# Performance work log

Measured on AMD Instinct MI355X. Metric: run time of the kernel, lower is better.

The kernel has to match this reference:

```python
import jax, jax.numpy as jnp
import numpy as np

K_NN = 10  # k in the source

def setup_inputs() -> dict:
    key = jax.random.key(0)
    k1, k2, k3, k4, k5 = jax.random.split(key, 5)
    bs, N, d, n_concepts, n_classes = 4096, 200000, 256, 32, 10
    return {
        "train_embedding": jax.random.normal(k1, (bs, d), dtype=jnp.float32),
        "train_embeddings": jax.random.normal(k2, (N, d), dtype=jnp.float32),
        # init_concept: uniform in [-0.5, 0.5]
        "concept": jax.random.uniform(k3, (d, n_concepts), dtype=jnp.float32, minval=-0.5, maxval=0.5),
        "W_hx": jax.random.normal(k4, (d, n_classes), dtype=jnp.float32) * 0.05,
        "b_hx": jax.random.normal(k5, (n_classes,), dtype=jnp.float32) * 0.05,
    }


def reference(train_embedding, train_embeddings, concept, W_hx, b_hx):
    # concept: [d, nc]; train_embeddings: [N, d]; train_embedding: [bs, d]
    n_concepts = concept.shape[1]

    def h_x(z):  # linear classifier standing in for h_x
        return z @ W_hx + b_hx

    gram = concept.T @ concept                                # [nc, nc]
    proj_matrix = concept @ jnp.linalg.inv(gram) @ concept.T  # [d, d]
    proj = train_embedding @ proj_matrix.T                    # (proj_matrix @ X^T)^T, [bs, d]
    y_pred = h_x(proj)
    orig_pred = h_x(train_embedding)

    # Batched cdist across all concepts (replaces the per-concept python loop):
    # dist[n, j] = || train_embeddings[n] - concept[:, j] ||
    x2 = jnp.sum(train_embeddings * train_embeddings, axis=1, keepdims=True)  # [N, 1]
    c2 = jnp.sum(concept * concept, axis=0)                                   # [nc]
    xc = train_embeddings @ concept                                           # [N, nc]
    dist = jnp.sqrt(jnp.maximum(x2 + c2 - 2.0 * xc, 0.0))                     # [N, nc]

    # top-k SMALLEST distances per concept
    _, knn_idx = jax.lax.top_k(-dist.T, K_NN)          # [nc, k]
    knn = train_embeddings[knn_idx]                    # [nc, k, d] gather

    # L_sparse_1: mean over concepts of sum(c * c_knn) / k
    dots = jnp.einsum("dj,jkd->j", concept, knn) / K_NN   # [nc]
    L_sparse_1_new = jnp.mean(dots)

    eye = jnp.eye(n_concepts, dtype=gram.dtype)
    L_sparse_2_new = jnp.mean(gram * (1.0 - eye))
    norm_metrics = jnp.mean(gram * eye)

    return (orig_pred, y_pred, L_sparse_1_new, L_sparse_2_new, norm_metrics)
```

## Files before the change

### kernel.cpp

```cpp
#include <hip/hip_runtime.h>
#include <cstdint>

#define D 256
#define NC 32
#define NCLS 10
#define KNN 10
#define KROWS 128
#define CTS 260

typedef float f32x4 __attribute__((ext_vector_type(4)));
typedef float f4v __attribute__((ext_vector_type(4)));
typedef short short8v __attribute__((ext_vector_type(8)));

__device__ __forceinline__ float wave_sum(float v) {
  #pragma unroll
  for (int off = 32; off; off >>= 1) v += __shfl_xor(v, off);
  return v;
}

__device__ __forceinline__ uint32_t fbits(float x) { return __builtin_bit_cast(uint32_t, x); }
__device__ __forceinline__ float bcast(uint32_t b) { return __builtin_bit_cast(float, b); }

__global__ __launch_bounds__(512, 4) void k_key(const float* __restrict__ X,
                                                const float* __restrict__ C,
                                                float* __restrict__ candK,
                                                int* __restrict__ candI,
                                                int N, int G) {
  __shared__ uint4 shm[2048];
  int t = threadIdx.x;
  int lane = t & 63;
  int wvu = __builtin_amdgcn_readfirstlane(t >> 6);
  int rowbase = blockIdx.x * KROWS;

  #pragma unroll
  for (int e0 = 0; e0 < 1024; e0 += 512) {
    int e = e0 + t;
    int q = e >> 6, l = e & 63;
    int tile = q >> 3, ksq = q & 7;
    int col = tile * 16 + (l & 15), kg = (l >> 4) & 3;
    uint32_t h[8], lo[8];
    #pragma unroll
    for (int i = 0; i < 8; ++i) {
      int k = ksq * 32 + kg * 8 + i;
      float x = C[(size_t)k * NC + col];
      uint32_t hb = fbits(x) & 0xFFFF0000u;
      h[i] = hb >> 16;
      lo[i] = fbits(x - bcast(hb)) >> 16;
    }
    shm[e] = make_uint4((h[1] << 16) | h[0], (h[3] << 16) | h[2],
                        (h[5] << 16) | h[4], (h[7] << 16) | h[6]);
    shm[1024 + e] = make_uint4((lo[1] << 16) | lo[0], (lo[3] << 16) | lo[2],
                               (lo[5] << 16) | lo[4], (lo[7] << 16) | lo[6]);
  }
  __syncthreads();

  int r16 = lane & 15;
  int grow = rowbase + wvu * 16 + r16; if (grow >= N) grow = N - 1;
  const float* xp = X + (size_t)grow * D + ((lane >> 4) * 8);

  f32x4 aH0, aM0, aH1, aM1;
  #pragma unroll
  for (int i = 0; i < 4; ++i) { aH0[i] = 0.f; aM0[i] = 0.f; aH1[i] = 0.f; aM1[i] = 0.f; }
  float x2 = 0.f;

  #pragma unroll
  for (int ks = 0; ks < 8; ++ks) {
    f4v xa = __builtin_nontemporal_load(reinterpret_cast<const f4v*>(xp + ks * 32));
    f4v xb = __builtin_nontemporal_load(reinterpret_cast<const f4v*>(xp + ks * 32 + 4));
    float xs[8] = {xa[0], xa[1], xa[2], xa[3], xb[0], xb[1], xb[2], xb[3]};
    uint32_t hp[4], lp[4];
    #pragma unroll
    for (int p = 0; p < 4; ++p) {
      float x0 = xs[2 * p], x1 = xs[2 * p + 1];
      x2 = fmaf(x0, x0, x2); x2 = fmaf(x1, x1, x2);
      uint32_t h0 = fbits(x0) & 0xFFFF0000u, h1 = fbits(x1) & 0xFFFF0000u;
      hp[p] = h1 | (h0 >> 16);
      float r0 = x0 - bcast(h0), r1 = x1 - bcast(h1);
      lp[p] = (fbits(r1) & 0xFFFF0000u) | (fbits(r0) >> 16);
    }
    short8v xh = __builtin_bit_cast(short8v, make_uint4(hp[0], hp[1], hp[2], hp[3]));
    short8v xl = __builtin_bit_cast(short8v, make_uint4(lp[0], lp[1], lp[2], lp[3]));
    short8v b0h = __builtin_bit_cast(short8v, shm[ks * 64 + lane]);
    short8v b1h = __builtin_bit_cast(short8v, shm[(8 + ks) * 64 + lane]);
    short8v b0l = __builtin_bit_cast(short8v, shm[1024 + ks * 64 + lane]);
    short8v b1l = __builtin_bit_cast(short8v, shm[1024 + (8 + ks) * 64 + lane]);
    aH0 = __builtin_amdgcn_mfma_f32_16x16x32_bf16(xh, b0h, aH0, 0, 0, 0);
    aM0 = __builtin_amdgcn_mfma_f32_16x16x32_bf16(xh, b0l, aM0, 0, 0, 0);
    aM0 = __builtin_amdgcn_mfma_f32_16x16x32_bf16(xl, b0h, aM0, 0, 0, 0);
    aH1 = __builtin_amdgcn_mfma_f32_16x16x32_bf16(xh, b1h, aH1, 0, 0, 0);
    aM1 = __builtin_amdgcn_mfma_f32_16x16x32_bf16(xh, b1l, aM1, 0, 0, 0);
    aM1 = __builtin_amdgcn_mfma_f32_16x16x32_bf16(xl, b1h, aM1, 0, 0, 0);
  }

  x2 += __shfl_xor(x2, 16);
  x2 += __shfl_xor(x2, 32);

  __syncthreads();
  float* klb = reinterpret_cast<float*>(shm);
  #pragma unroll
  for (int i = 0; i < 4; ++i) {
    int m = (lane >> 4) * 4 + i;
    float x2m = __shfl(x2, m);
    int rowl = wvu * 16 + m;
    klb[rowl * 33 + r16]      = fmaf(-2.f, aH0[i] + aM0[i], x2m);
    klb[rowl * 33 + 16 + r16] = fmaf(-2.f, aH1[i] + aM1[i], x2m);
  }
  __syncthreads();

  {
    int c = t >> 4, sub = t & 15;
    const float INF = 3.4e38f;
    float bk[8]; int bi[8];
    #pragma unroll
    for (int q = 0; q < 8; ++q) { bk[q] = INF; bi[q] = 0x7fffffff; }
    #pragma unroll
    for (int rr = 0; rr < 8; ++rr) {
      int rowl = sub * 8 + rr;
      int gi = rowbase + rowl;
      float v = (gi < N) ? klb[rowl * 33 + c] : INF;
      float cv = v; int ci = gi;
      #pragma unroll
      for (int q = 0; q < 8; ++q) {
        bool take = (cv < bk[q]) || (cv == bk[q] && ci < bi[q]);
        if (take) {
          float tf = bk[q]; bk[q] = cv; cv = tf;
          int ti = bi[q]; bi[q] = ci; ci = ti;
        }
      }
    }
    #pragma unroll
    for (int r = 0; r < KNN; ++r) {
      float mv = bk[0]; int mgi = bi[0];
      #pragma unroll
      for (int off = 1; off < 16; off <<= 1) {
        float ov = __shfl_xor(mv, off); int oi = __shfl_xor(mgi, off);
        if (ov < mv || (ov == mv && oi < mgi)) { mv = ov; mgi = oi; }
      }
      bool won = (bk[0] == mv) && (bi[0] == mgi);
      #pragma unroll
      for (int q = 0; q < 7; ++q) {
        bk[q] = won ? bk[q + 1] : bk[q];
        bi[q] = won ? bi[q + 1] : bi[q];
      }
      if (won) { bk[7] = INF; bi[7] = 0x7fffffff; }
      if (sub == 0) {
        candK[((size_t)c * G + blockIdx.x) * KNN + r] = mv;
        candI[((size_t)c * G + blockIdx.x) * KNN + r] = mgi;
      }
    }
  }
}

#define AUGW (NC + NCLS)
__global__ __launch_bounds__(1024) void k_gramsolve(const float* __restrict__ C,
                                                    const float* __restrict__ W,
                                                    float* __restrict__ T2,
                                                    float* __restrict__ out, int bs) {
  __shared__ float T[(NC + NCLS) * CTS];
  __shared__ float aug[NC * AUGW];
  __shared__ float Ssh[NC * NCLS];
  int tid = threadIdx.x;

  const float4* C4 = (const float4*)C;
  for (int s = tid; s < 2048; s += 1024) {
    float4 v = C4[s];
    int d = s >> 3, c0 = (s & 7) * 4;
    T[(c0 + 0) * CTS + d] = v.x; T[(c0 + 1) * CTS + d] = v.y;
    T[(c0 + 2) * CTS + d] = v.z; T[(c0 + 3) * CTS + d] = v.w;
  }
  const float2* W2 = (const float2*)W;
  for (int s = tid; s < 1280; s += 1024) {
    float2 v = W2[s];
    int d = s / 5, c0 = (s % 5) * 2;
    T[(NC + c0) * CTS + d] = v.x; T[(NC + c0 + 1) * CTS + d] = v.y;
  }
  __syncthreads();

  int lane = tid & 63, wv = tid >> 6;
  #pragma unroll
  for (int half = 0; half < 2; ++half) {
    int i = wv + half * 16;
    if (lane < AUGW) {
      const float4* ri = (const float4*)&T[i * CTS];
      const float4* rj = (const float4*)&T[lane * CTS];
      float acc = 0.f;
      #pragma unroll 8
      for (int d4 = 0; d4 < 64; ++d4) {
        float4 a = ri[d4], b = rj[d4];
        acc += a.x * b.x + a.y * b.y + a.z * b.z + a.w * b.w;
      }
      aug[i * AUGW + lane] = acc;
    }
  }
  __syncthreads();

  if (tid < NC) {
    int l2 = tid;
    float row[AUGW];
    #pragma unroll
    for (int c = 0; c < AUGW; ++c) row[c] = aug[l2 * AUGW + c];

    float rsum = 0.f;
    #pragma unroll
    for (int c = 0; c < NC; ++c) rsum += row[c];
    float diag = row[l2];
    #pragma unroll
    for (int off = 16; off; off >>= 1) {
      rsum += __shfl_xor(rsum, off);
      diag += __shfl_xor(diag, off);
    }
    if (l2 == 0) {
      out[(size_t)2 * bs * NCLS + 1] = (rsum - diag) / (float)(NC * NC);
      out[(size_t)2 * bs * NCLS + 2] = diag / (float)(NC * NC);
      out[(size_t)2 * bs * NCLS] = 0.f;
    }

    for (int k = 0; k < NC; ++k) {
      float prow[AUGW];
      #pragma unroll
      for (int c = 0; c < AUGW; ++c) prow[c] = __shfl(row[c], k);
      float pinv = 1.0f / prow[k];
      float f = row[k] * pinv;
      if (l2 == k) {
        #pragma unroll
        for (int c = 0; c < AUGW; ++c) row[c] *= pinv;
      } else {
        #pragma unroll
        for (int c = 0; c < AUGW; ++c) row[c] -= f * prow[c];
      }
    }
    #pragma unroll
    for (int c = 0; c < NCLS; ++c) Ssh[l2 * NCLS + c] = row[NC + c];
  }
  __syncthreads();

  for (int e = tid; e < D * NCLS; e += 1024) {
    int d = e / NCLS, cls = e % NCLS;
    float acc = 0.f;
    #pragma unroll
    for (int c = 0; c < NC; ++c) acc += T[c * CTS + d] * Ssh[c * NCLS + cls];
    T2[e] = acc;
  }
}

__global__ __launch_bounds__(256) void k_pred(const float* __restrict__ X,
                                              const float* __restrict__ W,
                                              const float* __restrict__ T2,
                                              const float* __restrict__ bvec,
                                              float* __restrict__ out, int bs) {
  __shared__ float2 Ws2[1280];
  __shared__ float2 Ts2[1280];
  int t = threadIdx.x;
  const float2* W2 = (const float2*)W;
  const float2* T22 = (const float2*)T2;
  for (int s = t; s < 1280; s += 256) { Ws2[s] = W2[s]; Ts2[s] = T22[s]; }
  __syncthreads();

  int r = blockIdx.x * 8 + (t >> 5);
  int q = t & 31;
  const float4* x4 = reinterpret_cast<const float4*>(X + (size_t)r * D);
  float4 xa = x4[q * 2], xb = x4[q * 2 + 1];

  float o[NCLS], y[NCLS];
  #pragma unroll
  for (int c = 0; c < NCLS; ++c) { o[c] = 0.f; y[c] = 0.f; }

  #pragma unroll
  for (int i = 0; i < 8; ++i) {
    int d = q * 8 + i;
    float xd = (i < 4) ? reinterpret_cast<const float*>(&xa)[i]
                       : reinterpret_cast<const float*>(&xb)[i - 4];
    #pragma unroll
    for (int j = 0; j < 5; ++j) {
      float2 wv = Ws2[d * 5 + j];
      float2 tv = Ts2[d * 5 + j];
      o[j * 2 + 0] += xd * wv.x; o[j * 2 + 1] += xd * wv.y;
      y[j * 2 + 0] += xd * tv.x; y[j * 2 + 1] += xd * tv.y;
    }
  }
  #pragma unroll
  for (int off = 1; off < 32; off <<= 1) {
    #pragma unroll
    for (int c = 0; c < NCLS; ++c) {
      o[c] += __shfl_xor(o[c], off);
      y[c] += __shfl_xor(y[c], off);
    }
  }
  if (q < NCLS) {
    float b = bvec[q];
    out[(size_t)r * NCLS + q] = o[q] + b;
    out[(size_t)bs * NCLS + (size_t)r * NCLS + q] = y[q] + b;
  }
}

__global__ __launch_bounds__(512) void k_final(const float* __restrict__ candK,
                                               const int* __restrict__ candI,
                                               const float* __restrict__ X,
                                               const float* __restrict__ Cc,
                                               float* __restrict__ out, int bs, int G) {
  int j = blockIdx.x, tid = threadIdx.x;
  int M = G * KNN;
  const float INF = 3.4e38f;

  float bk[KNN]; int bi[KNN];
  #pragma unroll
  for (int q = 0; q < KNN; ++q) { bk[q] = INF; bi[q] = 0x7fffffff; }
  for (int e = tid; e < M; e += 512) {
    float v = candK[(size_t)j * M + e];
    int gi = candI[(size_t)j * M + e];
    if (v < bk[KNN - 1] || (v == bk[KNN - 1] && gi < bi[KNN - 1])) {
      float cv = v; int ci = gi;
      #pragma unroll
      for (int q = 0; q < KNN; ++q) {
        bool take = (cv < bk[q]) || (cv == bk[q] && ci < bi[q]);
        if (take) {
          float tf = bk[q]; bk[q] = cv; cv = tf;
          int ti = bi[q]; bi[q] = ci; ci = ti;
        }
      }
    }
  }

  __shared__ float sk[512 * KNN];
  __shared__ int si[512 * KNN];
  __shared__ float wv_[8]; __shared__ int wi_[8];
  __shared__ int topIdx[KNN];
  #pragma unroll
  for (int q = 0; q < KNN; ++q) { sk[tid * KNN + q] = bk[q]; si[tid * KNN + q] = bi[q]; }
  __syncthreads();

  int p = 0;
  int lane = tid & 63, wv = tid >> 6;
  for (int rr = 0; rr < KNN; ++rr) {
    float myv = (p < KNN) ? sk[tid * KNN + p] : INF;
    int mygi = (p < KNN) ? si[tid * KNN + p] : 0x7fffffff;
    float hv = myv; int hgi = mygi;
    #pragma unroll
    for (int off = 32; off; off >>= 1) {
      float ov = __shfl_xor(hv, off); int oi = __shfl_xor(hgi, off);
      if (ov < hv || (ov == hv && oi < hgi)) { hv = ov; hgi = oi; }
    }
    if (lane == 0) { wv_[wv] = hv; wi_[wv] = hgi; }
    __syncthreads();
    float bv = wv_[0]; int bgi = wi_[0];
    #pragma unroll
    for (int w = 1; w < 8; ++w) {
      if (wv_[w] < bv || (wv_[w] == bv && wi_[w] < bgi)) { bv = wv_[w]; bgi = wi_[w]; }
    }
    if (p < KNN && myv == bv && mygi == bgi) p++;
    if (tid == 0) topIdx[rr] = bgi;
    __syncthreads();
  }

  if (tid < 256) {
    float cj = Cc[tid * NC + j];
    float acc = 0.f;
    #pragma unroll
    for (int k = 0; k < KNN; ++k) acc += X[(size_t)topIdx[k] * D + tid] * cj;
    acc = wave_sum(acc);
    __shared__ float rsum[4];
    if (lane == 0) rsum[wv] = acc;
    __syncthreads();
    if (tid == 0)
      atomicAdd(out + (size_t)2 * bs * NCLS,
                (rsum[0] + rsum[1] + rsum[2] + rsum[3]) * (1.0f / (KNN * NC)));
  }
}

extern "C" void kernel_launch(void* const* d_in, const int* in_sizes, int n_in,
                              void* d_out, int out_size, void* d_ws, size_t ws_size,
                              hipStream_t stream) {
  const float* Xb = (const float*)d_in[0];
  const float* XN = (const float*)d_in[1];
  const float* C  = (const float*)d_in[2];
  const float* W  = (const float*)d_in[3];
  const float* bv = (const float*)d_in[4];
  float* out = (float*)d_out;

  int bs = in_sizes[0] / D;
  int N  = in_sizes[1] / D;
  int G  = (N + KROWS - 1) / KROWS;

  float* w = (float*)d_ws;
  size_t offT2   = 0;
  size_t offCK   = 2560;
  size_t offCI   = offCK + (size_t)NC * G * KNN;

  float* T2    = w + offT2;
  float* candK = w + offCK;
  int*   candI = (int*)(w + offCI);

  k_key<<<dim3(G), dim3(512), 0, stream>>>(XN, C, candK, candI, N, G);
  k_gramsolve<<<dim3(1), dim3(1024), 0, stream>>>(C, W, T2, out, bs);
  k_pred<<<dim3(bs / 8), dim3(256), 0, stream>>>(Xb, W, T2, bv, out, bs);
  k_final<<<dim3(NC), dim3(512), 0, stream>>>(candK, candI, XN, C, out, bs, G);
}
```

Measured before the change: 165.3 us.

## Precompute concept bf16 split once and stage rows via async global-to-LDS loads

The bf16 hi/lo split of the concept matrix moves into the single-block gramsolve kernel, which now runs first and writes it to workspace. k_key loads it straight into registers instead of rebuilding it in every block. k_key now streams 32 rows per block into XOR-swizzled LDS with global_load_lds, and splits the 32 concept columns across wave pairs in 256-thread blocks. The candidate count rises to G≈6250 blocks with top-10 taken from 32 rows each, which enlarges the candidate lists the final kernel must merge. It also serialises gramsolve ahead of k_key.

```diff
diff --git a/kernel.cpp b/kernel.cpp
--- a/kernel.cpp
+++ b/kernel.cpp
@@ -5,12 +5,13 @@
 #define NC 32
 #define NCLS 10
 #define KNN 10
-#define KROWS 128
+#define KROWS 32
 #define CTS 260
 
 typedef float f32x4 __attribute__((ext_vector_type(4)));
-typedef float f4v __attribute__((ext_vector_type(4)));
 typedef short short8v __attribute__((ext_vector_type(8)));
+typedef const __attribute__((address_space(1))) unsigned int* gp1_t;
+typedef __attribute__((address_space(3))) unsigned int* sp3_t;
 
 __device__ __forceinline__ float wave_sum(float v) {
   #pragma unroll
@@ -21,53 +22,51 @@
 __device__ __forceinline__ uint32_t fbits(float x) { return __builtin_bit_cast(uint32_t, x); }
 __device__ __forceinline__ float bcast(uint32_t b) { return __builtin_bit_cast(float, b); }
 
-__global__ __launch_bounds__(512, 4) void k_key(const float* __restrict__ X,
-                                                const float* __restrict__ C,
+__global__ __launch_bounds__(256, 4) void k_key(const float* __restrict__ X,
+                                                const uint4* __restrict__ Fhi,
+                                                const uint4* __restrict__ Flo,
                                                 float* __restrict__ candK,
                                                 int* __restrict__ candI,
                                                 int N, int G) {
-  __shared__ uint4 shm[2048];
+  __shared__ float4 xf4[32 * 64];
   int t = threadIdx.x;
   int lane = t & 63;
   int wvu = __builtin_amdgcn_readfirstlane(t >> 6);
+  int tile = wvu & 1, rg = wvu >> 1;
   int rowbase = blockIdx.x * KROWS;
 
   #pragma unroll
-  for (int e0 = 0; e0 < 1024; e0 += 512) {
-    int e = e0 + t;
-    int q = e >> 6, l = e & 63;
-    int tile = q >> 3, ksq = q & 7;
-    int col = tile * 16 + (l & 15), kg = (l >> 4) & 3;
-    uint32_t h[8], lo[8];
-    #pragma unroll
-    for (int i = 0; i < 8; ++i) {
-      int k = ksq * 32 + kg * 8 + i;
-      float x = C[(size_t)k * NC + col];
-      uint32_t hb = fbits(x) & 0xFFFF0000u;
-      h[i] = hb >> 16;
-      lo[i] = fbits(x - bcast(hb)) >> 16;
-    }
-    shm[e] = make_uint4((h[1] << 16) | h[0], (h[3] << 16) | h[2],
-                        (h[5] << 16) | h[4], (h[7] << 16) | h[6]);
-    shm[1024 + e] = make_uint4((lo[1] << 16) | lo[0], (lo[3] << 16) | lo[2],
-                               (lo[5] << 16) | lo[4], (lo[7] << 16) | lo[6]);
-  }
-  __syncthreads();
-
-  int r16 = lane & 15;
-  int grow = rowbase + wvu * 16 + r16; if (grow >= N) grow = N - 1;
-  const float* xp = X + (size_t)grow * D + ((lane >> 4) * 8);
-
-  f32x4 aH0, aM0, aH1, aM1;
-  #pragma unroll
-  for (int i = 0; i < 4; ++i) { aH0[i] = 0.f; aM0[i] = 0.f; aH1[i] = 0.f; aM1[i] = 0.f; }
+  for (int j = 0; j < 8; ++j) {
+    int row = wvu * 8 + j;
+    int gr = rowbase + row; if (gr >= N) gr = N - 1;
+    const float* src = X + (size_t)gr * D + ((lane ^ (row & 15)) * 4);
+    __builtin_amdgcn_global_load_lds((gp1_t)(const void*)src,
+        (sp3_t)(void*)(&xf4[row * 64]), 16, 0, 0);
+  }
+
+  uint4 fh[8], fl[8];
+  #pragma unroll
+  for (int ks = 0; ks < 8; ++ks) {
+    fh[ks] = Fhi[(tile * 8 + ks) * 64 + lane];
+    fl[ks] = Flo[(tile * 8 + ks) * 64 + lane];
+  }
+
+  __syncthreads();
+
+  int r16 = lane & 15, kg = lane >> 4;
+  int rl = rg * 16 + r16;
+
+  f32x4 aH, aM;
+  #pragma unroll
+  for (int i = 0; i < 4; ++i) { aH[i] = 0.f; aM[i] = 0.f; }
   float x2 = 0.f;
 
   #pragma unroll
   for (int ks = 0; ks < 8; ++ks) {
-    f4v xa = __builtin_nontemporal_load(reinterpret_cast<const f4v*>(xp + ks * 32));
-    f4v xb = __builtin_nontemporal_load(reinterpret_cast<const f4v*>(xp + ks * 32 + 4));
-    float xs[8] = {xa[0], xa[1], xa[2], xa[3], xb[0], xb[1], xb[2], xb[3]};
+    int s0 = ks * 8 + kg * 2;
+    float4 xa = xf4[rl * 64 + (s0 ^ r16)];
+    float4 xb = xf4[rl * 64 + ((s0 + 1) ^ r16)];
+    float xs[8] = {xa.x, xa.y, xa.z, xa.w, xb.x, xb.y, xb.z, xb.w};
     uint32_t hp[4], lp[4];
     #pragma unroll
     for (int p = 0; p < 4; ++p) {
@@ -80,47 +79,41 @@
     }
     short8v xh = __builtin_bit_cast(short8v, make_uint4(hp[0], hp[1], hp[2], hp[3]));
     short8v xl = __builtin_bit_cast(short8v, make_uint4(lp[0], lp[1], lp[2], lp[3]));
-    short8v b0h = __builtin_bit_cast(short8v, shm[ks * 64 + lane]);
-    short8v b1h = __builtin_bit_cast(short8v, shm[(8 + ks) * 64 + lane]);
-    short8v b0l = __builtin_bit_cast(short8v, shm[1024 + ks * 64 + lane]);
-    short8v b1l = __builtin_bit_cast(short8v, shm[1024 + (8 + ks) * 64 + lane]);
-    aH0 = __builtin_amdgcn_mfma_f32_16x16x32_bf16(xh, b0h, aH0, 0, 0, 0);
-    aM0 = __builtin_amdgcn_mfma_f32_16x16x32_bf16(xh, b0l, aM0, 0, 0, 0);
-    aM0 = __builtin_amdgcn_mfma_f32_16x16x32_bf16(xl, b0h, aM0, 0, 0, 0);
-    aH1 = __builtin_amdgcn_mfma_f32_16x16x32_bf16(xh, b1h, aH1, 0, 0, 0);
-    aM1 = __builtin_amdgcn_mfma_f32_16x16x32_bf16(xh, b1l, aM1, 0, 0, 0);
-    aM1 = __builtin_amdgcn_mfma_f32_16x16x32_bf16(xl, b1h, aM1, 0, 0, 0);
+    short8v bh = __builtin_bit_cast(short8v, fh[ks]);
+    short8v bl = __builtin_bit_cast(short8v, fl[ks]);
+    aH = __builtin_amdgcn_mfma_f32_16x16x32_bf16(xh, bh, aH, 0, 0, 0);
+    aM = __builtin_amdgcn_mfma_f32_16x16x32_bf16(xh, bl, aM, 0, 0, 0);
+    aM = __builtin_amdgcn_mfma_f32_16x16x32_bf16(xl, bh, aM, 0, 0, 0);
   }
 
   x2 += __shfl_xor(x2, 16);
   x2 += __shfl_xor(x2, 32);
 
   __syncthreads();
-  float* klb = reinterpret_cast<float*>(shm);
+  float* klb = reinterpret_cast<float*>(xf4);
   #pragma unroll
   for (int i = 0; i < 4; ++i) {
     int m = (lane >> 4) * 4 + i;
     float x2m = __shfl(x2, m);
-    int rowl = wvu * 16 + m;
-    klb[rowl * 33 + r16]      = fmaf(-2.f, aH0[i] + aM0[i], x2m);
-    klb[rowl * 33 + 16 + r16] = fmaf(-2.f, aH1[i] + aM1[i], x2m);
+    int xrow = rg * 16 + m;
+    klb[xrow * 33 + tile * 16 + r16] = fmaf(-2.f, aH[i] + aM[i], x2m);
   }
   __syncthreads();
 
   {
-    int c = t >> 4, sub = t & 15;
+    int c = t >> 3, sub = t & 7;
     const float INF = 3.4e38f;
-    float bk[8]; int bi[8];
-    #pragma unroll
-    for (int q = 0; q < 8; ++q) { bk[q] = INF; bi[q] = 0x7fffffff; }
-    #pragma unroll
-    for (int rr = 0; rr < 8; ++rr) {
-      int rowl = sub * 8 + rr;
+    float bk[4]; int bi[4];
+    #pragma unroll
+    for (int q = 0; q < 4; ++q) { bk[q] = INF; bi[q] = 0x7fffffff; }
+    #pragma unroll
+    for (int rr = 0; rr < 4; ++rr) {
+      int rowl = sub * 4 + rr;
       int gi = rowbase + rowl;
       float v = (gi < N) ? klb[rowl * 33 + c] : INF;
       float cv = v; int ci = gi;
       #pragma unroll
-      for (int q = 0; q < 8; ++q) {
+      for (int q = 0; q < 4; ++q) {
         bool take = (cv < bk[q]) || (cv == bk[q] && ci < bi[q]);
         if (take) {
           float tf = bk[q]; bk[q] = cv; cv = tf;
@@ -132,17 +125,17 @@
     for (int r = 0; r < KNN; ++r) {
       float mv = bk[0]; int mgi = bi[0];
       #pragma unroll
-      for (int off = 1; off < 16; off <<= 1) {
+      for (int off = 1; off < 8; off <<= 1) {
         float ov = __shfl_xor(mv, off); int oi = __shfl_xor(mgi, off);
         if (ov < mv || (ov == mv && oi < mgi)) { mv = ov; mgi = oi; }
       }
       bool won = (bk[0] == mv) && (bi[0] == mgi);
       #pragma unroll
-      for (int q = 0; q < 7; ++q) {
+      for (int q = 0; q < 3; ++q) {
         bk[q] = won ? bk[q + 1] : bk[q];
         bi[q] = won ? bi[q + 1] : bi[q];
       }
-      if (won) { bk[7] = INF; bi[7] = 0x7fffffff; }
+      if (won) { bk[3] = INF; bi[3] = 0x7fffffff; }
       if (sub == 0) {
         candK[((size_t)c * G + blockIdx.x) * KNN + r] = mv;
         candI[((size_t)c * G + blockIdx.x) * KNN + r] = mgi;
@@ -154,12 +147,33 @@
 #define AUGW (NC + NCLS)
 __global__ __launch_bounds__(1024) void k_gramsolve(const float* __restrict__ C,
                                                     const float* __restrict__ W,
+                                                    uint4* __restrict__ Fhi,
+                                                    uint4* __restrict__ Flo,
                                                     float* __restrict__ T2,
                                                     float* __restrict__ out, int bs) {
+  int tid = threadIdx.x;
+  {
+    int l = tid & 63, q = tid >> 6;
+    int tile = q >> 3, ks = q & 7;
+    int col = tile * 16 + (l & 15), kg = (l >> 4) & 3;
+    uint32_t h[8], lo[8];
+    #pragma unroll
+    for (int i = 0; i < 8; ++i) {
+      int k = ks * 32 + kg * 8 + i;
+      float x = C[(size_t)k * NC + col];
+      uint32_t hb = fbits(x) & 0xFFFF0000u;
+      h[i] = hb >> 16;
+      lo[i] = fbits(x - bcast(hb)) >> 16;
+    }
+    Fhi[q * 64 + l] = make_uint4((h[1] << 16) | h[0], (h[3] << 16) | h[2],
+                                 (h[5] << 16) | h[4], (h[7] << 16) | h[6]);
+    Flo[q * 64 + l] = make_uint4((lo[1] << 16) | lo[0], (lo[3] << 16) | lo[2],
+                                 (lo[5] << 16) | lo[4], (lo[7] << 16) | lo[6]);
+  }
+
   __shared__ float T[(NC + NCLS) * CTS];
   __shared__ float aug[NC * AUGW];
   __shared__ float Ssh[NC * NCLS];
-  int tid = threadIdx.x;
 
   const float4* C4 = (const float4*)C;
   for (int s = tid; s < 2048; s += 1024) {
@@ -383,15 +397,19 @@
 
   float* w = (float*)d_ws;
   size_t offT2   = 0;
-  size_t offCK   = 2560;
+  size_t offFhi  = 2560;
+  size_t offFlo  = offFhi + 4096;
+  size_t offCK   = offFlo + 4096;
   size_t offCI   = offCK + (size_t)NC * G * KNN;
 
   float* T2    = w + offT2;
+  uint4* Fhi   = (uint4*)(w + offFhi);
+  uint4* Flo   = (uint4*)(w + offFlo);
   float* candK = w + offCK;
   int*   candI = (int*)(w + offCI);
 
-  k_key<<<dim3(G), dim3(512), 0, stream>>>(XN, C, candK, candI, N, G);
-  k_gramsolve<<<dim3(1), dim3(1024), 0, stream>>>(C, W, T2, out, bs);
+  k_gramsolve<<<dim3(1), dim3(1024), 0, stream>>>(C, W, Fhi, Flo, T2, out, bs);
+  k_key<<<dim3(G), dim3(256), 0, stream>>>(XN, Fhi, Flo, candK, candI, N, G);
   k_pred<<<dim3(bs / 8), dim3(256), 0, stream>>>(Xb, W, T2, bv, out, bs);
   k_final<<<dim3(NC), dim3(512), 0, stream>>>(candK, candI, XN, C, out, bs, G);
 }
```

After: 271.6 us. +64.3%, slower.

## Split final top-k merge into two-stage parallel reduction across partitions

Applied to the files above, without the earlier changes.

The single-pass final merge (one block per concept scanning all G*10 candidates) becomes two kernels. The first has 8 partition blocks per concept, each reducing its slice to a local top-10. The second merges the 80 survivors and computes the dot-product loss. This spreads the candidate scan over 256 blocks instead of 32, aimed at a serial tail that underused the GPU. The cost is an extra kernel launch and a small intermediate buffer.

```diff
diff --git a/kernel.cpp b/kernel.cpp
--- a/kernel.cpp
+++ b/kernel.cpp
@@ -7,6 +7,7 @@
 #define KNN 10
 #define KROWS 128
 #define CTS 260
+#define NPART 8
 
 typedef float f32x4 __attribute__((ext_vector_type(4)));
 typedef float f4v __attribute__((ext_vector_type(4)));
@@ -293,19 +294,53 @@
   }
 }
 
-__global__ __launch_bounds__(512) void k_final(const float* __restrict__ candK,
-                                               const int* __restrict__ candI,
-                                               const float* __restrict__ X,
-                                               const float* __restrict__ Cc,
-                                               float* __restrict__ out, int bs, int G) {
-  int j = blockIdx.x, tid = threadIdx.x;
+__device__ __forceinline__ void block_merge_top10(float* bk, int* bi, int tid,
+                                                  float* sk, int* si,
+                                                  float* wv_, int* wi_,
+                                                  float* outK, int* outI) {
+  const float INF = 3.4e38f;
+  #pragma unroll
+  for (int q = 0; q < KNN; ++q) { sk[tid * KNN + q] = bk[q]; si[tid * KNN + q] = bi[q]; }
+  __syncthreads();
+  int p = 0;
+  int lane = tid & 63, wv = tid >> 6;
+  for (int rr = 0; rr < KNN; ++rr) {
+    float myv = (p < KNN) ? sk[tid * KNN + p] : INF;
+    int mygi = (p < KNN) ? si[tid * KNN + p] : 0x7fffffff;
+    float hv = myv; int hgi = mygi;
+    #pragma unroll
+    for (int off = 32; off; off >>= 1) {
+      float ov = __shfl_xor(hv, off); int oi = __shfl_xor(hgi, off);
+      if (ov < hv || (ov == hv && oi < hgi)) { hv = ov; hgi = oi; }
+    }
+    if (lane == 0) { wv_[wv] = hv; wi_[wv] = hgi; }
+    __syncthreads();
+    float bv = wv_[0]; int bgi = wi_[0];
+    #pragma unroll
+    for (int w = 1; w < 4; ++w) {
+      if (wv_[w] < bv || (wv_[w] == bv && wi_[w] < bgi)) { bv = wv_[w]; bgi = wi_[w]; }
+    }
+    if (p < KNN && myv == bv && mygi == bgi) p++;
+    if (tid == 0) { outK[rr] = bv; outI[rr] = bgi; }
+    __syncthreads();
+  }
+}
+
+__global__ __launch_bounds__(256) void k_fmerge(const float* __restrict__ candK,
+                                                const int* __restrict__ candI,
+                                                float* __restrict__ c2K,
+                                                int* __restrict__ c2I, int G) {
+  int j = blockIdx.y, part = blockIdx.x, tid = threadIdx.x;
   int M = G * KNN;
+  int chunk = (M + NPART - 1) / NPART;
+  int lo = part * chunk;
+  int hi = lo + chunk; if (hi > M) hi = M;
   const float INF = 3.4e38f;
 
   float bk[KNN]; int bi[KNN];
   #pragma unroll
   for (int q = 0; q < KNN; ++q) { bk[q] = INF; bi[q] = 0x7fffffff; }
-  for (int e = tid; e < M; e += 512) {
+  for (int e = lo + tid; e < hi; e += 256) {
     float v = candK[(size_t)j * M + e];
     int gi = candI[(size_t)j * M + e];
     if (v < bk[KNN - 1] || (v == bk[KNN - 1] && gi < bi[KNN - 1])) {
@@ -321,50 +356,49 @@
     }
   }
 
-  __shared__ float sk[512 * KNN];
-  __shared__ int si[512 * KNN];
-  __shared__ float wv_[8]; __shared__ int wi_[8];
-  __shared__ int topIdx[KNN];
-  #pragma unroll
-  for (int q = 0; q < KNN; ++q) { sk[tid * KNN + q] = bk[q]; si[tid * KNN + q] = bi[q]; }
-  __syncthreads();
-
-  int p = 0;
+  __shared__ float sk[256 * KNN];
+  __shared__ int si[256 * KNN];
+  __shared__ float wv_[4]; __shared__ int wi_[4];
+  block_merge_top10(bk, bi, tid, sk, si, wv_, wi_,
+                    c2K + ((size_t)j * NPART + part) * KNN,
+                    c2I + ((size_t)j * NPART + part) * KNN);
+}
+
+__global__ __launch_bounds__(256) void k_final2(const float* __restrict__ c2K,
+                                                const int* __restrict__ c2I,
+                                                const float* __restrict__ X,
+                                                const float* __restrict__ Cc,
+                                                float* __restrict__ out, int bs) {
+  int j = blockIdx.x, tid = threadIdx.x;
+  const int M2 = NPART * KNN;
+  const float INF = 3.4e38f;
+
+  float bk[KNN]; int bi[KNN];
+  #pragma unroll
+  for (int q = 0; q < KNN; ++q) { bk[q] = INF; bi[q] = 0x7fffffff; }
+  if (tid < M2) {
+    bk[0] = c2K[(size_t)j * M2 + tid];
+    bi[0] = c2I[(size_t)j * M2 + tid];
+  }
+
+  __shared__ float sk[256 * KNN];
+  __shared__ int si[256 * KNN];
+  __shared__ float wv_[4]; __shared__ int wi_[4];
+  __shared__ float topK[KNN]; __shared__ int topIdx[KNN];
+  block_merge_top10(bk, bi, tid, sk, si, wv_, wi_, topK, topIdx);
+
   int lane = tid & 63, wv = tid >> 6;
-  for (int rr = 0; rr < KNN; ++rr) {
-    float myv = (p < KNN) ? sk[tid * KNN + p] : INF;
-    int mygi = (p < KNN) ? si[tid * KNN + p] : 0x7fffffff;
-    float hv = myv; int hgi = mygi;
-    #pragma unroll
-    for (int off = 32; off; off >>= 1) {
-      float ov = __shfl_xor(hv, off); int oi = __shfl_xor(hgi, off);
-      if (ov < hv || (ov == hv && oi < hgi)) { hv = ov; hgi = oi; }
-    }
-    if (lane == 0) { wv_[wv] = hv; wi_[wv] = hgi; }
-    __syncthreads();
-    float bv = wv_[0]; int bgi = wi_[0];
-    #pragma unroll
-    for (int w = 1; w < 8; ++w) {
-      if (wv_[w] < bv || (wv_[w] == bv && wi_[w] < bgi)) { bv = wv_[w]; bgi = wi_[w]; }
-    }
-    if (p < KNN && myv == bv && mygi == bgi) p++;
-    if (tid == 0) topIdx[rr] = bgi;
-    __syncthreads();
-  }
-
-  if (tid < 256) {
-    float cj = Cc[tid * NC + j];
-    float acc = 0.f;
-    #pragma unroll
-    for (int k = 0; k < KNN; ++k) acc += X[(size_t)topIdx[k] * D + tid] * cj;
-    acc = wave_sum(acc);
-    __shared__ float rsum[4];
-    if (lane == 0) rsum[wv] = acc;
-    __syncthreads();
-    if (tid == 0)
-      atomicAdd(out + (size_t)2 * bs * NCLS,
-                (rsum[0] + rsum[1] + rsum[2] + rsum[3]) * (1.0f / (KNN * NC)));
-  }
+  float cj = Cc[tid * NC + j];
+  float acc = 0.f;
+  #pragma unroll
+  for (int k = 0; k < KNN; ++k) acc += X[(size_t)topIdx[k] * D + tid] * cj;
+  acc = wave_sum(acc);
+  __shared__ float rsum[4];
+  if (lane == 0) rsum[wv] = acc;
+  __syncthreads();
+  if (tid == 0)
+    atomicAdd(out + (size_t)2 * bs * NCLS,
+              (rsum[0] + rsum[1] + rsum[2] + rsum[3]) * (1.0f / (KNN * NC)));
 }
 
 extern "C" void kernel_launch(void* const* d_in, const int* in_sizes, int n_in,
@@ -383,15 +417,20 @@
 
   float* w = (float*)d_ws;
   size_t offT2   = 0;
-  size_t offCK   = 2560;
+  size_t offC2K  = 2560;
+  size_t offC2I  = offC2K + NC * NPART * KNN;
+  size_t offCK   = offC2I + NC * NPART * KNN;
   size_t offCI   = offCK + (size_t)NC * G * KNN;
 
   float* T2    = w + offT2;
+  float* c2K   = w + offC2K;
+  int*   c2I   = (int*)(w + offC2I);
   float* candK = w + offCK;
   int*   candI = (int*)(w + offCI);
 
   k_key<<<dim3(G), dim3(512), 0, stream>>>(XN, C, candK, candI, N, G);
   k_gramsolve<<<dim3(1), dim3(1024), 0, stream>>>(C, W, T2, out, bs);
   k_pred<<<dim3(bs / 8), dim3(256), 0, stream>>>(Xb, W, T2, bv, out, bs);
-  k_final<<<dim3(NC), dim3(512), 0, stream>>>(candK, candI, XN, C, out, bs, G);
-}
+  k_fmerge<<<dim3(NPART, NC), dim3(256), 0, stream>>>(candK, candI, c2K, c2I, G);
+  k_final2<<<dim3(NC), dim3(256), 0, stream>>>(c2K, c2I, XN, C, out, bs);
+}
```

After: 146.2 us. 1.13x faster.
